# Kernel tuning notes

Measured on AMD Instinct MI355X. Metric: run time of the kernel, lower is better.

The kernel has to match this reference:

```python
import jax, jax.numpy as jnp
import numpy as np

B = 128          # batch
D = 2048         # original_dim
P = 16000        # projection_dim


def _count_sketch_matrix(key, d, p):
    """Dense count-sketch matrix: one +/-1 per row at a random column.
    Mirrors the torch init: col ~ randint(0, p-1), sign = 2*randint(0,2)-1."""
    k_idx, k_sgn = jax.random.split(key)
    idx = jax.random.randint(k_idx, (d,), 0, p - 1)            # torch uses high=p-1 (exclusive)
    sgn = (2 * jax.random.randint(k_sgn, (d,), 0, 2) - 1).astype(jnp.float32)
    C = jnp.zeros((d, p), dtype=jnp.float32)
    return C.at[jnp.arange(d), idx].set(sgn)


def setup_inputs() -> dict:
    key = jax.random.key(0)
    kx1, kx2, kc1, kc2 = jax.random.split(key, 4)
    x1 = jax.random.normal(kx1, (B, D), dtype=jnp.float32)
    x2 = jax.random.normal(kx2, (B, D), dtype=jnp.float32)
    C1 = _count_sketch_matrix(kc1, D, P)
    C2 = _count_sketch_matrix(kc2, D, P)
    return {"x1": x1, "x2": x2, "C1": C1, "C2": C2}


def reference(x1, x2, C1, C2):
    # Count-sketch projections (dense mm, as in the original module)
    y1 = x1 @ C1                      # [B, P]
    y2 = x2 @ C2                      # [B, P]
    # Circular convolution via FFT -> elementwise complex multiply -> IFFT.
    # Original takes only the real part of the IFFT output.
    f1 = jnp.fft.fft(y1, axis=-1)
    f2 = jnp.fft.fft(y2, axis=-1)
    phi = jnp.fft.ifft(f1 * f2, axis=-1).real.astype(jnp.float32)
    return phi                        # [B, P]
```

## Files before the change

### kernel.cpp

```cpp
#include <hip/hip_runtime.h>

#define NFFT 16000
#define BATCH 128
#define DIM 2048
#define TP 17

__device__ __forceinline__ float2 cmul(float2 a, float2 b) {
    return make_float2(a.x * b.x - a.y * b.y, a.x * b.y + a.y * b.x);
}
__device__ __forceinline__ float2 cadd(float2 a, float2 b) { return make_float2(a.x + b.x, a.y + b.y); }
__device__ __forceinline__ float2 csub(float2 a, float2 b) { return make_float2(a.x - b.x, a.y - b.y); }
__device__ __forceinline__ float2 cis(float ang) { return make_float2(__cosf(ang), __sinf(ang)); }

__device__ __forceinline__ int rev5_3(int n) {
    int d0 = n % 5, r = n / 5;
    int d1 = r % 5, d2 = r / 5;
    return d0 * 25 + d1 * 5 + d2;
}
__device__ __forceinline__ int rev7(int x) { return (int)(__brev((unsigned)x) >> 25); }

__device__ __forceinline__ float2 shfl2(float2 v, int lane) {
    return make_float2(__shfl(v.x, lane), __shfl(v.y, lane));
}

template<int CTRL>
__device__ __forceinline__ float dpp_mov(float v) {
    int i = __builtin_bit_cast(int, v);
    i = __builtin_amdgcn_update_dpp(i, i, CTRL, 0xF, 0xF, false);
    return __builtin_bit_cast(float, i);
}

#if __has_builtin(__builtin_amdgcn_permlane16_swap)
__device__ __forceinline__ float xchg16f(float v) {
    unsigned u = __builtin_bit_cast(unsigned, v);
    auto r = __builtin_amdgcn_permlane16_swap(u, u, false, false);
    return __builtin_bit_cast(float, (unsigned)(r[0] ^ r[1] ^ u));
}
#else
__device__ __forceinline__ float xchg16f(float v) { return __shfl_xor(v, 16); }
#endif

#if __has_builtin(__builtin_amdgcn_permlane32_swap)
__device__ __forceinline__ float xchg32f(float v) {
    unsigned u = __builtin_bit_cast(unsigned, v);
    auto r = __builtin_amdgcn_permlane32_swap(u, u, false, false);
    return __builtin_bit_cast(float, (unsigned)(r[0] ^ r[1] ^ u));
}
#else
__device__ __forceinline__ float xchg32f(float v) { return __shfl_xor(v, 32); }
#endif

template<int M>
__device__ __forceinline__ float xlane(float v) {
    if constexpr (M == 1)       return dpp_mov<0xB1>(v);
    else if constexpr (M == 2)  return dpp_mov<0x4E>(v);
    else if constexpr (M == 8)  return dpp_mov<0x128>(v);
    else if constexpr (M == 16) return xchg16f(v);
    else if constexpr (M == 32) return xchg32f(v);
    else                        return __shfl_xor(v, M);
}

__device__ __forceinline__ float2 conjG(float2 Zk, float2 Zm) {
    float u = (Zk.x * Zk.x - Zk.y * Zk.y) - (Zm.x * Zm.x - Zm.y * Zm.y);
    float v = 2.f * (Zk.x * Zk.y + Zm.x * Zm.y);
    return make_float2(0.25f * v, 0.25f * u);
}

template<int M>
__device__ __forceinline__ void dstage(float2& x0, float2& x1, float2 w, int l) {
    float2 o0 = make_float2(xlane<M>(x0.x), xlane<M>(x0.y));
    float2 o1 = make_float2(xlane<M>(x1.x), xlane<M>(x1.y));
    if (l & M) {
        x0 = cmul(csub(o0, x0), w);
        x1 = cmul(csub(o1, x1), w);
    } else {
        x0 = cadd(x0, o0);
        x1 = cadd(x1, o1);
    }
}

__device__ __forceinline__ void dif128(float2& x0, float2& x1, const float2* tw, int l) {
    {
        float2 a = x0, b = x1;
        x0 = cadd(a, b);
        x1 = cmul(csub(a, b), tw[0]);
    }
    dstage<32>(x0, x1, tw[1], l);
    dstage<16>(x0, x1, tw[2], l);
    dstage<8> (x0, x1, tw[3], l);
    dstage<4> (x0, x1, tw[4], l);
    dstage<2> (x0, x1, tw[5], l);
    dstage<1> (x0, x1, tw[6], l);
}

__global__ void extract_sketch(const float* __restrict__ C1, const float* __restrict__ C2,
                               int* __restrict__ idx1, float* __restrict__ sgn1,
                               int* __restrict__ idx2, float* __restrict__ sgn2) {
    int gwave = (blockIdx.x * blockDim.x + threadIdx.x) >> 6;
    int lane = threadIdx.x & 63;
    if (gwave >= 2 * DIM) return;
    const float* row;
    int* idxp; float* sgnp; int d;
    if (gwave < DIM) { d = gwave;       row = C1 + (size_t)d * NFFT; idxp = idx1; sgnp = sgn1; }
    else             { d = gwave - DIM; row = C2 + (size_t)d * NFFT; idxp = idx2; sgnp = sgn2; }

    float4 v[4], n[4];
    auto load_step = [&](float4* dst, int step) {
        int off0 = step * 1024 + lane * 4;
        #pragma unroll
        for (int c = 0; c < 4; ++c) {
            int off = off0 + c * 256;
            dst[c] = (off < NFFT) ? *reinterpret_cast<const float4*>(row + off)
                                  : make_float4(0.f, 0.f, 0.f, 0.f);
        }
    };
    load_step(v, 0);
    for (int step = 0; step < 16; ++step) {
        if (step + 1 < 16) load_step(n, step + 1);
        int off0 = step * 1024 + lane * 4;
        bool found = false;
        #pragma unroll
        for (int c = 0; c < 4; ++c) {
            float4 w = v[c];
            if (w.x != 0.f || w.y != 0.f || w.z != 0.f || w.w != 0.f) {
                int off = off0 + c * 256;
                int j; float s;
                if (w.x != 0.f)      { j = 0; s = w.x; }
                else if (w.y != 0.f) { j = 1; s = w.y; }
                else if (w.z != 0.f) { j = 2; s = w.z; }
                else                 { j = 3; s = w.w; }
                idxp[d] = off + j;
                sgnp[d] = s;
                found = true;
            }
        }
        if (__any(found)) return;
        #pragma unroll
        for (int c = 0; c < 4; ++c) v[c] = n[c];
    }
}

__global__ void __launch_bounds__(512) k1_colfft(
        const float* __restrict__ x1, const float* __restrict__ x2,
        const int* __restrict__ idx1, const float* __restrict__ sgn1,
        const int* __restrict__ idx2, const float* __restrict__ sgn2,
        float2* __restrict__ U) {
    __shared__ float2 S[32 * 125];
    const int b = blockIdx.x >> 2, q = blockIdx.x & 3;
    const int tid = threadIdx.x;

    for (int i = tid; i < 32 * 125; i += 512) S[i] = make_float2(0.f, 0.f);
    __syncthreads();

    const float* x1b = x1 + (size_t)b * DIM;
    const float* x2b = x2 + (size_t)b * DIM;
    for (int d = tid; d < DIM; d += 512) {
        int p1 = idx1[d]; int n1a = p1 & 127;
        if ((n1a >> 5) == q) atomicAdd(&S[(n1a & 31) * 125 + rev5_3(p1 >> 7)].x, sgn1[d] * x1b[d]);
        int p2 = idx2[d]; int n1b = p2 & 127;
        if ((n1b >> 5) == q) atomicAdd(&S[(n1b & 31) * 125 + rev5_3(p2 >> 7)].y, sgn2[d] * x2b[d]);
    }
    __syncthreads();

    const float C1_5 = 0.30901699437494742f, S1_5 = 0.95105651629515357f;
    const float C2_5 = -0.80901699437494745f, S2_5 = 0.58778525229247312f;
    const float2 w5tab[5] = { make_float2(1.f, 0.f),
                              make_float2(C1_5, -S1_5), make_float2(C2_5, -S2_5),
                              make_float2(C2_5,  S2_5), make_float2(C1_5,  S1_5) };
    #pragma unroll
    for (int s = 0; s < 3; ++s) {
        const int m = (s == 0) ? 1 : (s == 1) ? 5 : 25;
        const float angstep = -6.28318530717958647692f / (float)(5 * m);
        for (int task = tid; task < 32 * 25; task += 512) {
            int row = task / 25;
            int bf = task - row * 25;
            int t = bf % m, blk = bf / m;
            int base = row * 125 + blk * (5 * m) + t;
            float2 xv[5];
            #pragma unroll
            for (int r = 0; r < 5; ++r) xv[r] = S[base + r * m];
            if (m > 1) {
                float2 w1 = cis(angstep * (float)t);
                float2 w2 = cmul(w1, w1), w3 = cmul(w2, w1), w4 = cmul(w2, w2);
                xv[1] = cmul(xv[1], w1); xv[2] = cmul(xv[2], w2);
                xv[3] = cmul(xv[3], w3); xv[4] = cmul(xv[4], w4);
            }
            float2 y[5];
            #pragma unroll
            for (int qq = 0; qq < 5; ++qq) {
                float2 acc = xv[0];
                #pragma unroll
                for (int r = 1; r < 5; ++r) {
                    float2 t2 = cmul(xv[r], w5tab[(qq * r) % 5]);
                    acc.x += t2.x; acc.y += t2.y;
                }
                y[qq] = acc;
            }
            #pragma unroll
            for (int qq = 0; qq < 5; ++qq) S[base + qq * m] = y[qq];
        }
        __syncthreads();
    }

    const float ANGN = -6.28318530717958647692f / 16000.0f;
    const int n1base = q * 32;
    float2* Ub = U + (size_t)b * NFFT;
    for (int i = tid; i < 32 * 125; i += 512) {
        int n1l = i & 31, k2 = i >> 5;
        int n1 = n1base + n1l;
        Ub[k2 * 128 + n1] = cmul(S[n1l * 125 + k2], cis(ANGN * (float)(n1 * k2)));
    }
}

__global__ void __launch_bounds__(256) k2_pair(const float2* __restrict__ U,
                                               float2* __restrict__ V) {
    const int w = threadIdx.x >> 6, l = threadIdx.x & 63;
    const int task = blockIdx.x * 4 + w;
    const int b = task / 63, cg = task - b * 63;
    const int c = cg, cm = cg ? 125 - cg : 0;
    const float2* Ub = U + (size_t)b * NFFT;
    const float PI_F = 3.14159265358979323846f;

    float2 tw[7];
    tw[0] = cis(-PI_F / 64.0f * (float)l);
    {
        int m = 32;
        #pragma unroll
        for (int s = 1; s < 7; ++s, m >>= 1)
            tw[s] = cis(-PI_F / (float)m * (float)(l & (m - 1)));
    }

    float2 a0 = Ub[c * 128 + l], a1 = Ub[c * 128 + l + 64];
    dif128(a0, a1, tw, l);
    float2 b0, b1;
    if (cg) {
        b0 = Ub[cm * 128 + l]; b1 = Ub[cm * 128 + l + 64];
        dif128(b0, b1, tw, l);
    }

    const int e  = rev7(l);
    const int lp = rev7(126 - e);

    float2 gA0, gA1, gB0, gB1;
    if (cg) {
        float2 zm0 = shfl2(b1, lp);
        float2 zm1 = shfl2(b0, lp);
        gA0 = conjG(a0, zm0);
        gA1 = conjG(a1, zm1);
        float2 ym0 = shfl2(a1, lp);
        float2 ym1 = shfl2(a0, lp);
        gB0 = conjG(b0, ym0);
        gB1 = conjG(b1, ym1);
    } else {
        int hz = rev7((128 - e) & 127);
        float2 zm0 = shfl2(a0, hz);
        float2 zm1 = shfl2(a1, lp);
        gA0 = conjG(a0, zm0);
        gA1 = conjG(a1, zm1);
        gB0 = gB1 = make_float2(0.f, 0.f);
    }

    const int q = rev7(l & 62);
    const float ANGN = -6.28318530717958647692f / 16000.0f;
    float2* Vb = V + (size_t)b * NFFT;

    {
        float2 t00 = shfl2(gA0, q),     t10 = shfl2(gA1, q);
        float2 t01 = shfl2(gA0, q + 1), t11 = shfl2(gA1, q + 1);
        float2 p0 = (l & 1) ? t10 : t00;
        float2 p1 = (l & 1) ? t11 : t01;
        dif128(p0, p1, tw, l);
        p0 = cmul(p0, cis(ANGN * (float)(c * e)));
        p1 = cmul(p1, cis(ANGN * (float)(c * (e + 1))));
        *reinterpret_cast<float4*>(&Vb[c * 128 + e]) = make_float4(p0.x, p0.y, p1.x, p1.y);
    }
    if (cg) {
        float2 t00 = shfl2(gB0, q),     t10 = shfl2(gB1, q);
        float2 t01 = shfl2(gB0, q + 1), t11 = shfl2(gB1, q + 1);
        float2 p0 = (l & 1) ? t10 : t00;
        float2 p1 = (l & 1) ? t11 : t01;
        dif128(p0, p1, tw, l);
        p0 = cmul(p0, cis(ANGN * (float)(cm * e)));
        p1 = cmul(p1, cis(ANGN * (float)(cm * (e + 1))));
        *reinterpret_cast<float4*>(&Vb[cm * 128 + e]) = make_float4(p0.x, p0.y, p1.x, p1.y);
    }
}

__global__ void __launch_bounds__(256) k3_rowfft(const float2* __restrict__ V,
                                                 float* __restrict__ out) {
    __shared__ float2 T[125 * TP];
    const int b = blockIdx.x >> 3, g = blockIdx.x & 7;
    const int j1base = g * 16, tid = threadIdx.x;
    const float2* Vb = V + (size_t)b * NFFT;

    for (int i = tid; i < 125 * 16; i += 256) {
        int m1 = i >> 4, j1l = i & 15;
        T[rev5_3(m1) * TP + j1l] = Vb[m1 * 128 + j1base + j1l];
    }
    __syncthreads();

    const float C1_5 = 0.30901699437494742f, S1_5 = 0.95105651629515357f;
    const float C2_5 = -0.80901699437494745f, S2_5 = 0.58778525229247312f;
    const float2 w5tab[5] = { make_float2(1.f, 0.f),
                              make_float2(C1_5, -S1_5), make_float2(C2_5, -S2_5),
                              make_float2(C2_5,  S2_5), make_float2(C1_5,  S1_5) };
    #pragma unroll
    for (int s = 0; s < 3; ++s) {
        const int m = (s == 0) ? 1 : (s == 1) ? 5 : 25;
        const float angstep = -6.28318530717958647692f / (float)(5 * m);
        for (int task = tid; task < 16 * 25; task += 256) {
            int bf = task >> 4;
            int j1l = task & 15;
            int t = bf % m, blk = bf / m;
            int base = (blk * (5 * m) + t) * TP + j1l;
            float2 xv[5];
            #pragma unroll
            for (int r = 0; r < 5; ++r) xv[r] = T[base + r * m * TP];
            if (m > 1) {
                float2 w1 = cis(angstep * (float)t);
                float2 w2 = cmul(w1, w1), w3 = cmul(w2, w1), w4 = cmul(w2, w2);
                xv[1] = cmul(xv[1], w1); xv[2] = cmul(xv[2], w2);
                xv[3] = cmul(xv[3], w3); xv[4] = cmul(xv[4], w4);
            }
            float2 y[5];
            #pragma unroll
            for (int qq = 0; qq < 5; ++qq) {
                float2 acc = xv[0];
                #pragma unroll
                for (int r = 1; r < 5; ++r) {
                    float2 t2 = cmul(xv[r], w5tab[(qq * r) % 5]);
                    acc.x += t2.x; acc.y += t2.y;
                }
                y[qq] = acc;
            }
            #pragma unroll
            for (int qq = 0; qq < 5; ++qq) T[base + qq * m * TP] = y[qq];
        }
        __syncthreads();
    }

    const float invN = 1.0f / (float)NFFT;
    float* outb = out + (size_t)b * NFFT;
    for (int i = tid; i < 125 * 16; i += 256) {
        int j2 = i >> 4, j1l = i & 15;
        outb[j1base + j1l + 128 * j2] = T[j2 * TP + j1l].x * invN;
    }
}

extern "C" void kernel_launch(void* const* d_in, const int* in_sizes, int n_in,
                              void* d_out, int out_size, void* d_ws, size_t ws_size,
                              hipStream_t stream) {
    (void)in_sizes; (void)n_in; (void)out_size; (void)ws_size;
    const float* x1 = (const float*)d_in[0];
    const float* x2 = (const float*)d_in[1];
    const float* C1 = (const float*)d_in[2];
    const float* C2 = (const float*)d_in[3];
    float* out = (float*)d_out;

    char* w = (char*)d_ws;
    int*    idx1 = (int*)  (w);
    float*  sgn1 = (float*)(w + 8192);
    int*    idx2 = (int*)  (w + 16384);
    float*  sgn2 = (float*)(w + 24576);
    float2* U    = (float2*)(w + 32768);
    float2* V    = (float2*)(w + 32768 + 16384000);

    extract_sketch<<<(2 * DIM) / 4, 256, 0, stream>>>(C1, C2, idx1, sgn1, idx2, sgn2);
    k1_colfft     <<<BATCH * 4, 512, 0, stream>>>(x1, x2, idx1, sgn1, idx2, sgn2, U);
    k2_pair       <<<2016, 256, 0, stream>>>(U, V);
    k3_rowfft     <<<BATCH * 8, 256, 0, stream>>>(V, out);
}
```

Baseline: 297.1 us.

## Fuse four FFT stages into one cooperative persistent kernel with grid syncs

Replaces the four separate launches (sketch extraction, column FFT, pair/row FFT, final radix-5 row FFT) with a single cooperative kernel of 256 blocks × 1024 threads that separates the phases with grid.sync. The aim is to remove launch overhead and inter-kernel gaps. In exchange, each phase must now be remapped onto a fixed grid with different parallelism: the column FFT is split in halves across block pairs, and the final stage packs four tasks per block. That remapping can lower occupancy or balance, and each grid-wide barrier has its own cost. If the cooperative launch fails, it falls back to the old four-kernel path.

```diff
diff --git a/kernel.cpp b/kernel.cpp
--- a/kernel.cpp
+++ b/kernel.cpp
@@ -1,4 +1,7 @@
 #include <hip/hip_runtime.h>
+#include <hip/hip_cooperative_groups.h>
+
+namespace coopg = cooperative_groups;
 
 #define NFFT 16000
 #define BATCH 128
@@ -92,6 +95,7 @@
     dstage<2> (x0, x1, tw[5], l);
     dstage<1> (x0, x1, tw[6], l);
 }
+
 
 __global__ void extract_sketch(const float* __restrict__ C1, const float* __restrict__ C2,
                                int* __restrict__ idx1, float* __restrict__ sgn1,
@@ -216,8 +220,8 @@
                                                float2* __restrict__ V) {
     const int w = threadIdx.x >> 6, l = threadIdx.x & 63;
     const int task = blockIdx.x * 4 + w;
-    const int b = task / 63, cg = task - b * 63;
-    const int c = cg, cm = cg ? 125 - cg : 0;
+    const int b = task / 63, cp = task - b * 63;
+    const int c = cp, cm = cp ? 125 - cp : 0;
     const float2* Ub = U + (size_t)b * NFFT;
     const float PI_F = 3.14159265358979323846f;
 
@@ -233,7 +237,7 @@
     float2 a0 = Ub[c * 128 + l], a1 = Ub[c * 128 + l + 64];
     dif128(a0, a1, tw, l);
     float2 b0, b1;
-    if (cg) {
+    if (cp) {
         b0 = Ub[cm * 128 + l]; b1 = Ub[cm * 128 + l + 64];
         dif128(b0, b1, tw, l);
     }
@@ -242,7 +246,7 @@
     const int lp = rev7(126 - e);
 
     float2 gA0, gA1, gB0, gB1;
-    if (cg) {
+    if (cp) {
         float2 zm0 = shfl2(b1, lp);
         float2 zm1 = shfl2(b0, lp);
         gA0 = conjG(a0, zm0);
@@ -274,7 +278,7 @@
         p1 = cmul(p1, cis(ANGN * (float)(c * (e + 1))));
         *reinterpret_cast<float4*>(&Vb[c * 128 + e]) = make_float4(p0.x, p0.y, p1.x, p1.y);
     }
-    if (cg) {
+    if (cp) {
         float2 t00 = shfl2(gB0, q),     t10 = shfl2(gB1, q);
         float2 t01 = shfl2(gB0, q + 1), t11 = shfl2(gB1, q + 1);
         float2 p0 = (l & 1) ? t10 : t00;
@@ -347,6 +351,273 @@
     }
 }
 
+__global__ void __launch_bounds__(1024, 4) mega_fft(
+        const float* __restrict__ x1, const float* __restrict__ x2,
+        const float* __restrict__ C1, const float* __restrict__ C2,
+        int* __restrict__ idx1, float* __restrict__ sgn1,
+        int* __restrict__ idx2, float* __restrict__ sgn2,
+        float2* __restrict__ U, float2* __restrict__ V,
+        float* __restrict__ out) {
+    coopg::grid_group grid = coopg::this_grid();
+    __shared__ __align__(16) char smraw[4 * 125 * TP * sizeof(float2)];
+    float2* S = reinterpret_cast<float2*>(smraw);
+
+    const int tid = threadIdx.x;
+    const int wv = tid >> 6, l = tid & 63;
+    const int gw = (int)blockIdx.x * 16 + wv;
+
+    {
+        const float* rowp; int* idxp; float* sgnp; int d;
+        if (gw < DIM) { d = gw;       rowp = C1 + (size_t)d * NFFT; idxp = idx1; sgnp = sgn1; }
+        else          { d = gw - DIM; rowp = C2 + (size_t)d * NFFT; idxp = idx2; sgnp = sgn2; }
+
+        float4 v[4], nb[4];
+        auto load_step = [&](float4* dst, int step) {
+            int off0 = step * 1024 + l * 4;
+            #pragma unroll
+            for (int c = 0; c < 4; ++c) {
+                int off = off0 + c * 256;
+                dst[c] = (off < NFFT) ? *reinterpret_cast<const float4*>(rowp + off)
+                                      : make_float4(0.f, 0.f, 0.f, 0.f);
+            }
+        };
+        load_step(v, 0);
+        bool done = false;
+        for (int step = 0; step < 16 && !done; ++step) {
+            if (step + 1 < 16) load_step(nb, step + 1);
+            int off0 = step * 1024 + l * 4;
+            bool found = false;
+            #pragma unroll
+            for (int c = 0; c < 4; ++c) {
+                float4 ww = v[c];
+                if (ww.x != 0.f || ww.y != 0.f || ww.z != 0.f || ww.w != 0.f) {
+                    int off = off0 + c * 256;
+                    int j; float s;
+                    if (ww.x != 0.f)      { j = 0; s = ww.x; }
+                    else if (ww.y != 0.f) { j = 1; s = ww.y; }
+                    else if (ww.z != 0.f) { j = 2; s = ww.z; }
+                    else                  { j = 3; s = ww.w; }
+                    idxp[d] = off + j;
+                    sgnp[d] = s;
+                    found = true;
+                }
+            }
+            done = __any(found);
+            if (!done) {
+                #pragma unroll
+                for (int c = 0; c < 4; ++c) v[c] = nb[c];
+            }
+        }
+    }
+    __threadfence();
+    grid.sync();
+    __threadfence();
+
+    {
+        const int b = (int)blockIdx.x >> 1, h = (int)blockIdx.x & 1;
+        for (int i = tid; i < 64 * 125; i += 1024) S[i] = make_float2(0.f, 0.f);
+        __syncthreads();
+
+        const float* x1b = x1 + (size_t)b * DIM;
+        const float* x2b = x2 + (size_t)b * DIM;
+        for (int d = tid; d < DIM; d += 1024) {
+            int p1 = idx1[d]; int n1a = p1 & 127;
+            if ((n1a >> 6) == h) atomicAdd(&S[(n1a & 63) * 125 + rev5_3(p1 >> 7)].x, sgn1[d] * x1b[d]);
+            int p2 = idx2[d]; int n1b = p2 & 127;
+            if ((n1b >> 6) == h) atomicAdd(&S[(n1b & 63) * 125 + rev5_3(p2 >> 7)].y, sgn2[d] * x2b[d]);
+        }
+        __syncthreads();
+
+        const float C1_5 = 0.30901699437494742f, S1_5 = 0.95105651629515357f;
+        const float C2_5 = -0.80901699437494745f, S2_5 = 0.58778525229247312f;
+        const float2 w5tab[5] = { make_float2(1.f, 0.f),
+                                  make_float2(C1_5, -S1_5), make_float2(C2_5, -S2_5),
+                                  make_float2(C2_5,  S2_5), make_float2(C1_5,  S1_5) };
+        #pragma unroll
+        for (int s = 0; s < 3; ++s) {
+            const int m = (s == 0) ? 1 : (s == 1) ? 5 : 25;
+            const float angstep = -6.28318530717958647692f / (float)(5 * m);
+            for (int task = tid; task < 64 * 25; task += 1024) {
+                int row = task / 25;
+                int bf = task - row * 25;
+                int t = bf % m, blk = bf / m;
+                int base = row * 125 + blk * (5 * m) + t;
+                float2 xv[5];
+                #pragma unroll
+                for (int r = 0; r < 5; ++r) xv[r] = S[base + r * m];
+                if (m > 1) {
+                    float2 w1 = cis(angstep * (float)t);
+                    float2 w2 = cmul(w1, w1), w3 = cmul(w2, w1), w4 = cmul(w2, w2);
+                    xv[1] = cmul(xv[1], w1); xv[2] = cmul(xv[2], w2);
+                    xv[3] = cmul(xv[3], w3); xv[4] = cmul(xv[4], w4);
+                }
+                float2 y[5];
+                #pragma unroll
+                for (int qq = 0; qq < 5; ++qq) {
+                    float2 acc = xv[0];
+                    #pragma unroll
+                    for (int r = 1; r < 5; ++r) {
+                        float2 t2 = cmul(xv[r], w5tab[(qq * r) % 5]);
+                        acc.x += t2.x; acc.y += t2.y;
+                    }
+                    y[qq] = acc;
+                }
+                #pragma unroll
+                for (int qq = 0; qq < 5; ++qq) S[base + qq * m] = y[qq];
+            }
+            __syncthreads();
+        }
+
+        const float ANGN = -6.28318530717958647692f / 16000.0f;
+        float2* Ub = U + (size_t)b * NFFT;
+        for (int i = tid; i < 64 * 125; i += 1024) {
+            int n1l = i & 63, k2 = i >> 6;
+            int n1 = h * 64 + n1l;
+            Ub[k2 * 128 + n1] = cmul(S[n1l * 125 + k2], cis(ANGN * (float)(n1 * k2)));
+        }
+    }
+    __threadfence();
+    grid.sync();
+    __threadfence();
+
+    {
+        const float PI_F = 3.14159265358979323846f;
+        const float ANGN = -6.28318530717958647692f / 16000.0f;
+        float2 tw[7];
+        tw[0] = cis(-PI_F / 64.0f * (float)l);
+        {
+            int m = 32;
+            #pragma unroll
+            for (int s = 1; s < 7; ++s, m >>= 1)
+                tw[s] = cis(-PI_F / (float)m * (float)(l & (m - 1)));
+        }
+
+        for (int task = gw; task < 8064; task += 4096) {
+            const int b = task / 63, cp = task - b * 63;
+            const int c = cp, cm = cp ? 125 - cp : 0;
+            const float2* Ub = U + (size_t)b * NFFT;
+
+            float2 a0 = Ub[c * 128 + l], a1 = Ub[c * 128 + l + 64];
+            dif128(a0, a1, tw, l);
+            float2 b0, b1;
+            if (cp) {
+                b0 = Ub[cm * 128 + l]; b1 = Ub[cm * 128 + l + 64];
+                dif128(b0, b1, tw, l);
+            }
+
+            const int e  = rev7(l);
+            const int lp = rev7(126 - e);
+
+            float2 gA0, gA1, gB0, gB1;
+            if (cp) {
+                float2 zm0 = shfl2(b1, lp);
+                float2 zm1 = shfl2(b0, lp);
+                gA0 = conjG(a0, zm0);
+                gA1 = conjG(a1, zm1);
+                float2 ym0 = shfl2(a1, lp);
+                float2 ym1 = shfl2(a0, lp);
+                gB0 = conjG(b0, ym0);
+                gB1 = conjG(b1, ym1);
+            } else {
+                int hz = rev7((128 - e) & 127);
+                float2 zm0 = shfl2(a0, hz);
+                float2 zm1 = shfl2(a1, lp);
+                gA0 = conjG(a0, zm0);
+                gA1 = conjG(a1, zm1);
+                gB0 = gB1 = make_float2(0.f, 0.f);
+            }
+
+            const int q = rev7(l & 62);
+            float2* Vb = V + (size_t)b * NFFT;
+            {
+                float2 t00 = shfl2(gA0, q),     t10 = shfl2(gA1, q);
+                float2 t01 = shfl2(gA0, q + 1), t11 = shfl2(gA1, q + 1);
+                float2 p0 = (l & 1) ? t10 : t00;
+                float2 p1 = (l & 1) ? t11 : t01;
+                dif128(p0, p1, tw, l);
+                p0 = cmul(p0, cis(ANGN * (float)(c * e)));
+                p1 = cmul(p1, cis(ANGN * (float)(c * (e + 1))));
+                *reinterpret_cast<float4*>(&Vb[c * 128 + e]) = make_float4(p0.x, p0.y, p1.x, p1.y);
+            }
+            if (cp) {
+                float2 t00 = shfl2(gB0, q),     t10 = shfl2(gB1, q);
+                float2 t01 = shfl2(gB0, q + 1), t11 = shfl2(gB1, q + 1);
+                float2 p0 = (l & 1) ? t10 : t00;
+                float2 p1 = (l & 1) ? t11 : t01;
+                dif128(p0, p1, tw, l);
+                p0 = cmul(p0, cis(ANGN * (float)(cm * e)));
+                p1 = cmul(p1, cis(ANGN * (float)(cm * (e + 1))));
+                *reinterpret_cast<float4*>(&Vb[cm * 128 + e]) = make_float4(p0.x, p0.y, p1.x, p1.y);
+            }
+        }
+    }
+    __threadfence();
+    grid.sync();
+    __threadfence();
+
+    {
+        const int t4 = tid >> 8, st = tid & 255;
+        const int task = (int)blockIdx.x * 4 + t4;
+        const int b = task >> 3, g = task & 7;
+        float2* T = reinterpret_cast<float2*>(smraw) + t4 * 125 * TP;
+        const int j1base = g * 16;
+        const float2* Vb = V + (size_t)b * NFFT;
+
+        for (int i = st; i < 125 * 16; i += 256) {
+            int m1 = i >> 4, j1l = i & 15;
+            T[rev5_3(m1) * TP + j1l] = Vb[m1 * 128 + j1base + j1l];
+        }
+        __syncthreads();
+
+        const float C1_5 = 0.30901699437494742f, S1_5 = 0.95105651629515357f;
+        const float C2_5 = -0.80901699437494745f, S2_5 = 0.58778525229247312f;
+        const float2 w5tab[5] = { make_float2(1.f, 0.f),
+                                  make_float2(C1_5, -S1_5), make_float2(C2_5, -S2_5),
+                                  make_float2(C2_5,  S2_5), make_float2(C1_5,  S1_5) };
+        #pragma unroll
+        for (int s = 0; s < 3; ++s) {
+            const int m = (s == 0) ? 1 : (s == 1) ? 5 : 25;
+            const float angstep = -6.28318530717958647692f / (float)(5 * m);
+            for (int task5 = st; task5 < 16 * 25; task5 += 256) {
+                int bf = task5 >> 4;
+                int j1l = task5 & 15;
+                int t = bf % m, blk = bf / m;
+                int base = (blk * (5 * m) + t) * TP + j1l;
+                float2 xv[5];
+                #pragma unroll
+                for (int r = 0; r < 5; ++r) xv[r] = T[base + r * m * TP];
+                if (m > 1) {
+                    float2 w1 = cis(angstep * (float)t);
+                    float2 w2 = cmul(w1, w1), w3 = cmul(w2, w1), w4 = cmul(w2, w2);
+                    xv[1] = cmul(xv[1], w1); xv[2] = cmul(xv[2], w2);
+                    xv[3] = cmul(xv[3], w3); xv[4] = cmul(xv[4], w4);
+                }
+                float2 y[5];
+                #pragma unroll
+                for (int qq = 0; qq < 5; ++qq) {
+                    float2 acc = xv[0];
+                    #pragma unroll
+                    for (int r = 1; r < 5; ++r) {
+                        float2 t2 = cmul(xv[r], w5tab[(qq * r) % 5]);
+                        acc.x += t2.x; acc.y += t2.y;
+                    }
+                    y[qq] = acc;
+                }
+                #pragma unroll
+                for (int qq = 0; qq < 5; ++qq) T[base + qq * m * TP] = y[qq];
+            }
+            __syncthreads();
+        }
+
+        const float invN = 1.0f / (float)NFFT;
+        float* outb = out + (size_t)b * NFFT;
+        for (int i = st; i < 125 * 16; i += 256) {
+            int j2 = i >> 4, j1l = i & 15;
+            outb[j1base + j1l + 128 * j2] = T[j2 * TP + j1l].x * invN;
+        }
+    }
+}
+
 extern "C" void kernel_launch(void* const* d_in, const int* in_sizes, int n_in,
                               void* d_out, int out_size, void* d_ws, size_t ws_size,
                               hipStream_t stream) {
@@ -365,8 +636,15 @@
     float2* U    = (float2*)(w + 32768);
     float2* V    = (float2*)(w + 32768 + 16384000);
 
-    extract_sketch<<<(2 * DIM) / 4, 256, 0, stream>>>(C1, C2, idx1, sgn1, idx2, sgn2);
-    k1_colfft     <<<BATCH * 4, 512, 0, stream>>>(x1, x2, idx1, sgn1, idx2, sgn2, U);
-    k2_pair       <<<2016, 256, 0, stream>>>(U, V);
-    k3_rowfft     <<<BATCH * 8, 256, 0, stream>>>(V, out);
-}
+    void* args[] = { (void*)&x1, (void*)&x2, (void*)&C1, (void*)&C2,
+                     (void*)&idx1, (void*)&sgn1, (void*)&idx2, (void*)&sgn2,
+                     (void*)&U, (void*)&V, (void*)&out };
+    hipError_t e = hipLaunchCooperativeKernel(reinterpret_cast<const void*>(&mega_fft),
+                                              dim3(256), dim3(1024), args, 0u, stream);
+    if (e != hipSuccess) {
+        extract_sketch<<<(2 * DIM) / 4, 256, 0, stream>>>(C1, C2, idx1, sgn1, idx2, sgn2);
+        k1_colfft     <<<BATCH * 4, 512, 0, stream>>>(x1, x2, idx1, sgn1, idx2, sgn2, U);
+        k2_pair       <<<2016, 256, 0, stream>>>(U, V);
+        k3_rowfft     <<<BATCH * 8, 256, 0, stream>>>(V, out);
+    }
+}
```

After: 947.0 us. +218.7%, slower.
